# Performance work log

Measured on AMD Instinct MI355X. Metric: run time of the kernel, lower is better.

## Reference

```python
import jax, jax.numpy as jnp
import numpy as np

HIDDEN = 2048
N_HEADS = 16
Q_DIM = N_HEADS * 128  # 2048
INTER = 10944
EPS = 1e-6
B, S = 2, 2048


def rms_norm(x, w, eps):
    var = jnp.mean(jnp.square(x), axis=-1, keepdims=True)
    return x * jax.lax.rsqrt(var + eps) * w


def setup_inputs() -> dict:
    key = jax.random.key(0)
    ks = jax.random.split(key, 8)
    x = jax.random.normal(ks[0], (B, S, HIDDEN), dtype=jnp.float32)
    positions = jnp.broadcast_to(jnp.arange(S, dtype=jnp.int32), (B, S))
    sc = 0.02
    return {
        "x": x,
        "positions": positions,
        "in_w": jnp.ones((HIDDEN,), dtype=jnp.float32),
        "post_w": jnp.ones((HIDDEN,), dtype=jnp.float32),
        "Wq": jax.random.normal(ks[1], (Q_DIM, HIDDEN), dtype=jnp.float32) * sc,
        "Wo": jax.random.normal(ks[2], (HIDDEN, Q_DIM), dtype=jnp.float32) * sc,
        "Wg": jax.random.normal(ks[3], (INTER, HIDDEN), dtype=jnp.float32) * sc,
        "Wu": jax.random.normal(ks[4], (INTER, HIDDEN), dtype=jnp.float32) * sc,
        "Wd": jax.random.normal(ks[5], (HIDDEN, INTER), dtype=jnp.float32) * sc,
    }


def reference(x, positions, in_w, post_w, Wq, Wo, Wg, Wu, Wd):
    b, s, h = x.shape
    xf = x.reshape(-1, h)                       # [T, H]
    h_norm = rms_norm(xf, in_w, EPS)            # RMSNorm (input_layernorm)
    q = jnp.einsum('th,qh->tq', h_norm, Wq)     # q_proj
    hidden = xf + jnp.einsum('tq,hq->th', q, Wo)  # o_proj + residual
    h_post = rms_norm(hidden, post_w, EPS)      # post_attention_layernorm
    gate = jax.nn.silu(jnp.einsum('th,ih->ti', h_post, Wg))
    up = jnp.einsum('th,ih->ti', h_post, Wu)
    mlp = jnp.einsum('ti,hi->th', gate * up, Wd)  # down_proj
    return (hidden + mlp).reshape(b, s, h)
```

## Files before the change

kernel.cpp:

```cpp
#include <hip/hip_runtime.h>
#include <hip/hip_bf16.h>
#include <stdint.h>


typedef __bf16 bf16;
typedef bf16 bf16x8 __attribute__((ext_vector_type(8)));
typedef bf16 bf16x4 __attribute__((ext_vector_type(4)));
typedef float f32x4 __attribute__((ext_vector_type(4)));

#define HID     2048
#define TOK     4096
#define INTER   10944
#define INTER_P 11008
#define BK      32

__device__ __forceinline__ void gload_lds16(const bf16* g, bf16* l) {
    __builtin_amdgcn_global_load_lds(
        (const __attribute__((address_space(1))) void*)g,
        (__attribute__((address_space(3))) void*)l, 16, 0, 0);
}

__global__ __launch_bounds__(256) void conv_pad(const float* __restrict__ src,
                                                bf16* __restrict__ dst,
                                                int n_src, int n_dst) {
    int i = (blockIdx.x * 256 + threadIdx.x) * 4;
    if (i >= n_dst) return;
    float4 v = make_float4(0.f, 0.f, 0.f, 0.f);
    if (i < n_src) v = *(const float4*)(src + i);
    bf16x4 o;
    o[0] = (bf16)v.x; o[1] = (bf16)v.y; o[2] = (bf16)v.z; o[3] = (bf16)v.w;
    *(bf16x4*)(dst + i) = o;
}

__global__ __launch_bounds__(256) void conv_wd(const float* __restrict__ src,
                                               bf16* __restrict__ dst) {
    int i = (blockIdx.x * 256 + threadIdx.x) * 4;
    if (i >= HID * INTER_P) return;
    int row = i / INTER_P;
    int col = i - row * INTER_P;
    float4 v = make_float4(0.f, 0.f, 0.f, 0.f);
    if (col < INTER)
        v = *(const float4*)(src + (size_t)row * INTER + col);
    bf16x4 o;
    o[0] = (bf16)v.x; o[1] = (bf16)v.y; o[2] = (bf16)v.z; o[3] = (bf16)v.w;
    *(bf16x4*)(dst + i) = o;
}

__global__ __launch_bounds__(256) void rmsnorm_k(const float* __restrict__ x,
                                                 const float* __restrict__ w,
                                                 bf16* __restrict__ out) {
    const int row = blockIdx.x;
    const int tid = threadIdx.x;
    const float* xr = x + (size_t)row * HID + tid * 8;
    float4 v0 = *(const float4*)(xr);
    float4 v1 = *(const float4*)(xr + 4);
    float s = v0.x * v0.x + v0.y * v0.y + v0.z * v0.z + v0.w * v0.w +
              v1.x * v1.x + v1.y * v1.y + v1.z * v1.z + v1.w * v1.w;
    #pragma unroll
    for (int o = 32; o > 0; o >>= 1) s += __shfl_down(s, o);
    __shared__ float red[4];
    if ((tid & 63) == 0) red[tid >> 6] = s;
    __syncthreads();
    float tot = red[0] + red[1] + red[2] + red[3];
    float scale = rsqrtf(tot * (1.0f / (float)HID) + 1e-6f);
    float4 w0 = *(const float4*)(w + tid * 8);
    float4 w1 = *(const float4*)(w + tid * 8 + 4);
    bf16x8 o8;
    o8[0] = (bf16)(v0.x * scale * w0.x);
    o8[1] = (bf16)(v0.y * scale * w0.y);
    o8[2] = (bf16)(v0.z * scale * w0.z);
    o8[3] = (bf16)(v0.w * scale * w0.w);
    o8[4] = (bf16)(v1.x * scale * w1.x);
    o8[5] = (bf16)(v1.y * scale * w1.y);
    o8[6] = (bf16)(v1.z * scale * w1.z);
    o8[7] = (bf16)(v1.w * scale * w1.w);
    *(bf16x8*)(out + (size_t)row * HID + tid * 8) = o8;
}

template <int EPI>
__global__ __launch_bounds__(512, 4) void gemm_bt5(const bf16* __restrict__ A,
                                                   const bf16* __restrict__ W,
                                                   const float* __restrict__ res,
                                                   void* __restrict__ out,
                                                   int N, int K) {
    __shared__ bf16 lA[128 * BK];
    __shared__ bf16 lW[128 * BK];
    const int tid = threadIdx.x;
    const int rowBase = blockIdx.x * 128;
    const int colBase = blockIdx.y * 128;
    const int wave = tid >> 6, lane = tid & 63;
    const int wm = (wave >> 2) * 64, wn = (wave & 3) * 32;
    const int lr = lane & 15, kq = lane >> 4;

    f32x4 acc[4][2] = {};
    const bf16* Ab = A + (size_t)rowBase * K;
    const bf16* Wb = W + (size_t)colBase * K;

    const int sr = tid >> 2;
    const int ss = (tid & 3) ^ ((sr >> 1) & 3);
    const size_t goff = (size_t)sr * K + ss * 8;

    int aoff[4], woff[2];
    #pragma unroll
    for (int i = 0; i < 4; ++i) {
        int r = wm + i * 16 + lr;
        aoff[i] = r * BK + (kq ^ ((r >> 1) & 3)) * 8;
    }
    #pragma unroll
    for (int i = 0; i < 2; ++i) {
        int r = wn + i * 16 + lr;
        woff[i] = r * BK + (kq ^ ((r >> 1) & 3)) * 8;
    }

    for (int k0 = 0; k0 < K; k0 += BK) {
        gload_lds16(Ab + goff + k0, &lA[tid * 8]);
        gload_lds16(Wb + goff + k0, &lW[tid * 8]);
        __syncthreads();
        bf16x8 af[4], wf[2];
        #pragma unroll
        for (int i = 0; i < 4; ++i) af[i] = *(const bf16x8*)&lA[aoff[i]];
        #pragma unroll
        for (int i = 0; i < 2; ++i) wf[i] = *(const bf16x8*)&lW[woff[i]];
        #pragma unroll
        for (int mi = 0; mi < 4; ++mi)
            #pragma unroll
            for (int ni = 0; ni < 2; ++ni)
                acc[mi][ni] = __builtin_amdgcn_mfma_f32_16x16x32_bf16(
                    af[mi], wf[ni], acc[mi][ni], 0, 0, 0);
        __syncthreads();
    }
    const int rq = lane >> 4, cn = lane & 15;
    #pragma unroll
    for (int mi = 0; mi < 4; ++mi) {
        #pragma unroll
        for (int ni = 0; ni < 2; ++ni) {
            int col = colBase + wn + ni * 16 + cn;
            #pragma unroll
            for (int r = 0; r < 4; ++r) {
                int row = rowBase + wm + mi * 16 + rq * 4 + r;
                size_t idx = (size_t)row * N + col;
                float v = acc[mi][ni][r];
                if (EPI == 0) ((bf16*)out)[idx] = (bf16)v;
                else          ((float*)out)[idx] = res[idx] + v;
            }
        }
    }
}

__global__ __launch_bounds__(512, 4) void gemm_gu5(const bf16* __restrict__ A,
                                                   const bf16* __restrict__ Wg,
                                                   const bf16* __restrict__ Wu,
                                                   bf16* __restrict__ out,
                                                   int N, int K) {
    __shared__ bf16 lA[128 * BK];
    __shared__ bf16 lG[128 * BK];
    __shared__ bf16 lU[128 * BK];
    const int tid = threadIdx.x;
    const int rowBase = blockIdx.x * 128;
    const int colBase = blockIdx.y * 128;
    const int wave = tid >> 6, lane = tid & 63;
    const int wm = (wave >> 2) * 64, wn = (wave & 3) * 32;
    const int lr = lane & 15, kq = lane >> 4;

    f32x4 ag[4][2] = {};
    f32x4 au[4][2] = {};
    const bf16* Ab = A + (size_t)rowBase * K;
    const bf16* Gb = Wg + (size_t)colBase * K;
    const bf16* Ub = Wu + (size_t)colBase * K;

    const int sr = tid >> 2;
    const int ss = (tid & 3) ^ ((sr >> 1) & 3);
    const size_t goff = (size_t)sr * K + ss * 8;

    int aoff[4], boff[2];
    #pragma unroll
    for (int i = 0; i < 4; ++i) {
        int r = wm + i * 16 + lr;
        aoff[i] = r * BK + (kq ^ ((r >> 1) & 3)) * 8;
    }
    #pragma unroll
    for (int i = 0; i < 2; ++i) {
        int r = wn + i * 16 + lr;
        boff[i] = r * BK + (kq ^ ((r >> 1) & 3)) * 8;
    }

    for (int k0 = 0; k0 < K; k0 += BK) {
        gload_lds16(Ab + goff + k0, &lA[tid * 8]);
        gload_lds16(Gb + goff + k0, &lG[tid * 8]);
        gload_lds16(Ub + goff + k0, &lU[tid * 8]);
        __syncthreads();
        bf16x8 af[4], gf[2], uf[2];
        #pragma unroll
        for (int i = 0; i < 4; ++i) af[i] = *(const bf16x8*)&lA[aoff[i]];
        #pragma unroll
        for (int i = 0; i < 2; ++i) {
            gf[i] = *(const bf16x8*)&lG[boff[i]];
            uf[i] = *(const bf16x8*)&lU[boff[i]];
        }
        #pragma unroll
        for (int mi = 0; mi < 4; ++mi)
            #pragma unroll
            for (int ni = 0; ni < 2; ++ni) {
                ag[mi][ni] = __builtin_amdgcn_mfma_f32_16x16x32_bf16(
                    af[mi], gf[ni], ag[mi][ni], 0, 0, 0);
                au[mi][ni] = __builtin_amdgcn_mfma_f32_16x16x32_bf16(
                    af[mi], uf[ni], au[mi][ni], 0, 0, 0);
            }
        __syncthreads();
    }
    const int rq = lane >> 4, cn = lane & 15;
    #pragma unroll
    for (int mi = 0; mi < 4; ++mi) {
        #pragma unroll
        for (int ni = 0; ni < 2; ++ni) {
            int col = colBase + wn + ni * 16 + cn;
            #pragma unroll
            for (int r = 0; r < 4; ++r) {
                int row = rowBase + wm + mi * 16 + rq * 4 + r;
                float g = ag[mi][ni][r];
                float u = au[mi][ni][r];
                float sg = g / (1.0f + __expf(-g));
                out[(size_t)row * N + col] = (bf16)(sg * u);
            }
        }
    }
}

extern "C" void kernel_launch(void* const* d_in, const int* in_sizes, int n_in,
                              void* d_out, int out_size, void* d_ws, size_t ws_size,
                              hipStream_t stream) {
    const float* x      = (const float*)d_in[0];
    const float* in_w   = (const float*)d_in[2];
    const float* post_w = (const float*)d_in[3];
    const float* Wq     = (const float*)d_in[4];
    const float* Wo     = (const float*)d_in[5];
    const float* Wg     = (const float*)d_in[6];
    const float* Wu     = (const float*)d_in[7];
    const float* Wd     = (const float*)d_in[8];

    char* ws = (char*)d_ws;
    bf16*  X    = (bf16*)(ws + 0);
    bf16*  Yq   = (bf16*)(ws + 16777216);
    float* hid  = (float*)(ws + 33554432);
    bf16*  gu   = (bf16*)(ws + 67108864);
    bf16*  w0   = (bf16*)(ws + 157286400);
    bf16*  w1   = (bf16*)(ws + 202375168);
    bf16*  wsm  = (bf16*)(ws + 247463936);

    const int nGU  = INTER_P * HID;
    const int nGUs = INTER * HID;
    const int nSq  = HID * HID;

    conv_pad<<<nGU / 4 / 256, 256, 0, stream>>>(Wg, w0, nGUs, nGU);
    conv_pad<<<nGU / 4 / 256, 256, 0, stream>>>(Wu, w1, nGUs, nGU);
    conv_pad<<<nSq / 4 / 256, 256, 0, stream>>>(Wq, wsm, nSq, nSq);

    rmsnorm_k<<<TOK, 256, 0, stream>>>(x, in_w, X);
    gemm_bt5<0><<<dim3(TOK / 128, HID / 128), 512, 0, stream>>>(
        X, wsm, nullptr, Yq, HID, HID);
    conv_pad<<<nSq / 4 / 256, 256, 0, stream>>>(Wo, wsm, nSq, nSq);
    gemm_bt5<1><<<dim3(TOK / 128, HID / 128), 512, 0, stream>>>(
        Yq, wsm, x, hid, HID, HID);
    rmsnorm_k<<<TOK, 256, 0, stream>>>(hid, post_w, X);
    gemm_gu5<<<dim3(TOK / 128, INTER_P / 128), 512, 0, stream>>>(
        X, w0, w1, gu, INTER_P, HID);
    conv_wd<<<nGU / 4 / 256, 256, 0, stream>>>(Wd, w0);
    gemm_bt5<1><<<dim3(TOK / 128, HID / 128), 512, 0, stream>>>(
        gu, w0, hid, (float*)d_out, HID, INTER_P);
}
```

Baseline: 1.093 ms.

## Replace GEMMs with 256x256 double-buffered pipelined kernel plus split-K and combine passes

```diff
diff --git a/kernel.cpp b/kernel.cpp
--- a/kernel.cpp
+++ b/kernel.cpp
@@ -12,13 +12,19 @@
 #define TOK     4096
 #define INTER   10944
 #define INTER_P 11008
-#define BK      32
 
 __device__ __forceinline__ void gload_lds16(const bf16* g, bf16* l) {
     __builtin_amdgcn_global_load_lds(
         (const __attribute__((address_space(1))) void*)g,
         (__attribute__((address_space(3))) void*)l, 16, 0, 0);
 }
+
+#define SBAR()      asm volatile("s_barrier" ::: "memory")
+#define VMCNT(n)    asm volatile("s_waitcnt vmcnt(" #n ")" ::: "memory")
+#define LGKM(n)     asm volatile("s_waitcnt lgkmcnt(" #n ")" ::: "memory")
+#define SCHED0()    __builtin_amdgcn_sched_barrier(0)
+#define PRIO(n)     __builtin_amdgcn_s_setprio(n)
+#define FMA16(d, a, b) d = __builtin_amdgcn_mfma_f32_16x16x32_bf16(a, b, d, 0, 0, 0)
 
 __global__ __launch_bounds__(256) void conv_pad(const float* __restrict__ src,
                                                 bf16* __restrict__ dst,
@@ -77,151 +83,181 @@
     *(bf16x8*)(out + (size_t)row * HID + tid * 8) = o8;
 }
 
+#define BUFE 32768
+
 template <int EPI>
-__global__ __launch_bounds__(512, 4) void gemm_bt5(const bf16* __restrict__ A,
-                                                   const bf16* __restrict__ W,
-                                                   const float* __restrict__ res,
-                                                   void* __restrict__ out,
-                                                   int N, int K) {
-    __shared__ bf16 lA[128 * BK];
-    __shared__ bf16 lW[128 * BK];
+__global__ __launch_bounds__(512, 2) void gemm256(const bf16* __restrict__ A,
+                                                  const bf16* __restrict__ W,
+                                                  float* __restrict__ out0,
+                                                  float* __restrict__ out1,
+                                                  int N, int K, int ntz) {
+    extern __shared__ bf16 lds[];
     const int tid = threadIdx.x;
-    const int rowBase = blockIdx.x * 128;
-    const int colBase = blockIdx.y * 128;
+    const int rowBase = blockIdx.x * 256;
+    const int colBase = blockIdx.y * 256;
+    const int kt0 = blockIdx.z * ntz;
     const int wave = tid >> 6, lane = tid & 63;
-    const int wm = (wave >> 2) * 64, wn = (wave & 3) * 32;
-    const int lr = lane & 15, kq = lane >> 4;
-
-    f32x4 acc[4][2] = {};
-    const bf16* Ab = A + (size_t)rowBase * K;
-    const bf16* Wb = W + (size_t)colBase * K;
-
-    const int sr = tid >> 2;
-    const int ss = (tid & 3) ^ ((sr >> 1) & 3);
-    const size_t goff = (size_t)sr * K + ss * 8;
-
-    int aoff[4], woff[2];
+    const int wm = wave >> 2, wn = wave & 3;
+    const int fr = lane & 15, kq = lane >> 4;
+
+    const int slr = tid >> 3;
+    const int sc  = (tid & 7) ^ (slr & 7);
+    const bf16* sAb = A + (size_t)(rowBase + slr) * K + sc * 8;
+    const bf16* sWb = W + (size_t)(colBase + slr) * K + sc * 8;
+    const int ldst = tid * 8;
+
+    int aof[8][2], wof[4][2];
     #pragma unroll
-    for (int i = 0; i < 4; ++i) {
-        int r = wm + i * 16 + lr;
-        aoff[i] = r * BK + (kq ^ ((r >> 1) & 3)) * 8;
+    for (int mi = 0; mi < 8; ++mi) {
+        const int ra = mi * 32 + wm * 16 + fr;
+        #pragma unroll
+        for (int ks = 0; ks < 2; ++ks)
+            aof[mi][ks] = ra * 64 + (((ks * 4 + kq) ^ (ra & 7)) * 8);
     }
     #pragma unroll
-    for (int i = 0; i < 2; ++i) {
-        int r = wn + i * 16 + lr;
-        woff[i] = r * BK + (kq ^ ((r >> 1) & 3)) * 8;
+    for (int nj = 0; nj < 4; ++nj) {
+        const int rw = nj * 64 + wn * 16 + fr;
+        #pragma unroll
+        for (int ks = 0; ks < 2; ++ks)
+            wof[nj][ks] = 16384 + rw * 64 + (((ks * 4 + kq) ^ (rw & 7)) * 8);
     }
 
-    for (int k0 = 0; k0 < K; k0 += BK) {
-        gload_lds16(Ab + goff + k0, &lA[tid * 8]);
-        gload_lds16(Wb + goff + k0, &lW[tid * 8]);
-        __syncthreads();
-        bf16x8 af[4], wf[2];
-        #pragma unroll
-        for (int i = 0; i < 4; ++i) af[i] = *(const bf16x8*)&lA[aoff[i]];
-        #pragma unroll
-        for (int i = 0; i < 2; ++i) wf[i] = *(const bf16x8*)&lW[woff[i]];
-        #pragma unroll
-        for (int mi = 0; mi < 4; ++mi)
+    f32x4 acc[8][4] = {};
+
+#define STG(isA, hh, tt)                                                     \
+    do {                                                                     \
+        const bf16* _b = (isA) ? sAb : sWb;                                  \
+        bf16* _d = &lds[(((tt) & 1) * BUFE) + ((isA) ? 0 : 16384) +          \
+                        (hh) * 8192 + ldst];                                 \
+        const size_t _kb = (size_t)(kt0 + (tt)) * 64;                        \
+        gload_lds16(_b + (size_t)((hh) * 128) * K + _kb, _d);                \
+        gload_lds16(_b + (size_t)((hh) * 128 + 64) * K + _kb, _d + 4096);    \
+    } while (0)
+
+    STG(1, 0, 0); STG(0, 0, 0); STG(1, 1, 0); STG(0, 1, 0);
+    STG(1, 0, 1);
+    VMCNT(2);
+    SBAR();
+
+    for (int t = 0; t < ntz; ++t) {
+        const int bb = (t & 1) * BUFE;
+        const bool s1 = (t + 1) < ntz;
+        const bool s2 = (t + 2) < ntz;
+        bf16x8 aF[4][2], wF0[2][2], wF1[2][2];
+        if (s1) STG(0, 0, t + 1);
+        #pragma unroll
+        for (int m = 0; m < 4; ++m)
+          #pragma unroll
+          for (int ks = 0; ks < 2; ++ks)
+            aF[m][ks] = *(const bf16x8*)&lds[bb + aof[m][ks]];
+        #pragma unroll
+        for (int n = 0; n < 2; ++n)
+          #pragma unroll
+          for (int ks = 0; ks < 2; ++ks)
+            wF0[n][ks] = *(const bf16x8*)&lds[bb + wof[n][ks]];
+        LGKM(8);
+        SBAR(); LGKM(0); SCHED0();
+        PRIO(1);
+        #pragma unroll
+        for (int ks = 0; ks < 2; ++ks)
+          #pragma unroll
+          for (int m = 0; m < 4; ++m)
             #pragma unroll
-            for (int ni = 0; ni < 2; ++ni)
-                acc[mi][ni] = __builtin_amdgcn_mfma_f32_16x16x32_bf16(
-                    af[mi], wf[ni], acc[mi][ni], 0, 0, 0);
-        __syncthreads();
+            for (int n = 0; n < 2; ++n)
+                FMA16(acc[m][n], aF[m][ks], wF0[n][ks]);
+        PRIO(0); SCHED0(); SBAR();
+        if (s1) STG(1, 1, t + 1);
+        #pragma unroll
+        for (int n = 0; n < 2; ++n)
+          #pragma unroll
+          for (int ks = 0; ks < 2; ++ks)
+            wF1[n][ks] = *(const bf16x8*)&lds[bb + wof[2 + n][ks]];
+        SBAR(); LGKM(0); SCHED0();
+        PRIO(1);
+        #pragma unroll
+        for (int ks = 0; ks < 2; ++ks)
+          #pragma unroll
+          for (int m = 0; m < 4; ++m)
+            #pragma unroll
+            for (int n = 0; n < 2; ++n)
+                FMA16(acc[m][2 + n], aF[m][ks], wF1[n][ks]);
+        PRIO(0); SCHED0(); SBAR();
+        if (s1) STG(0, 1, t + 1);
+        #pragma unroll
+        for (int m = 0; m < 4; ++m)
+          #pragma unroll
+          for (int ks = 0; ks < 2; ++ks)
+            aF[m][ks] = *(const bf16x8*)&lds[bb + aof[4 + m][ks]];
+        SBAR(); LGKM(0); SCHED0();
+        PRIO(1);
+        #pragma unroll
+        for (int ks = 0; ks < 2; ++ks)
+          #pragma unroll
+          for (int m = 0; m < 4; ++m)
+            #pragma unroll
+            for (int n = 0; n < 2; ++n)
+                FMA16(acc[4 + m][2 + n], aF[m][ks], wF1[n][ks]);
+        PRIO(0); SCHED0(); SBAR();
+        if (s2) STG(1, 0, t + 2);
+        SCHED0();
+        PRIO(1);
+        #pragma unroll
+        for (int ks = 0; ks < 2; ++ks)
+          #pragma unroll
+          for (int m = 0; m < 4; ++m)
+            #pragma unroll
+            for (int n = 0; n < 2; ++n)
+                FMA16(acc[4 + m][n], aF[m][ks], wF0[n][ks]);
+        PRIO(0); SCHED0();
+        if (s2) VMCNT(2); else VMCNT(0);
+        SBAR();
     }
+#undef STG
     const int rq = lane >> 4, cn = lane & 15;
+    float* dst = blockIdx.z ? out1 : out0;
     #pragma unroll
-    for (int mi = 0; mi < 4; ++mi) {
-        #pragma unroll
-        for (int ni = 0; ni < 2; ++ni) {
-            int col = colBase + wn + ni * 16 + cn;
-            #pragma unroll
-            for (int r = 0; r < 4; ++r) {
-                int row = rowBase + wm + mi * 16 + rq * 4 + r;
-                size_t idx = (size_t)row * N + col;
-                float v = acc[mi][ni][r];
-                if (EPI == 0) ((bf16*)out)[idx] = (bf16)v;
-                else          ((float*)out)[idx] = res[idx] + v;
+    for (int mi = 0; mi < 8; ++mi)
+      #pragma unroll
+      for (int nj = 0; nj < 4; ++nj) {
+        const int col = colBase + nj * 64 + wn * 16 + cn;
+        #pragma unroll
+        for (int r = 0; r < 4; ++r) {
+            const int row = rowBase + mi * 32 + wm * 16 + rq * 4 + r;
+            const size_t idx = (size_t)row * N + col;
+            const float v = acc[mi][nj][r];
+            if (EPI == 0) {
+                dst[idx] = v;
+            } else if (EPI == 1) {
+                ((bf16*)out0)[idx] = (bf16)v;
+            } else {
+                bf16* p = (bf16*)out0;
+                const float u = (float)p[idx];
+                const float sg = v / (1.0f + __expf(-v));
+                p[idx] = (bf16)(sg * u);
             }
         }
-    }
-}
-
-__global__ __launch_bounds__(512, 4) void gemm_gu5(const bf16* __restrict__ A,
-                                                   const bf16* __restrict__ Wg,
-                                                   const bf16* __restrict__ Wu,
-                                                   bf16* __restrict__ out,
-                                                   int N, int K) {
-    __shared__ bf16 lA[128 * BK];
-    __shared__ bf16 lG[128 * BK];
-    __shared__ bf16 lU[128 * BK];
-    const int tid = threadIdx.x;
-    const int rowBase = blockIdx.x * 128;
-    const int colBase = blockIdx.y * 128;
-    const int wave = tid >> 6, lane = tid & 63;
-    const int wm = (wave >> 2) * 64, wn = (wave & 3) * 32;
-    const int lr = lane & 15, kq = lane >> 4;
-
-    f32x4 ag[4][2] = {};
-    f32x4 au[4][2] = {};
-    const bf16* Ab = A + (size_t)rowBase * K;
-    const bf16* Gb = Wg + (size_t)colBase * K;
-    const bf16* Ub = Wu + (size_t)colBase * K;
-
-    const int sr = tid >> 2;
-    const int ss = (tid & 3) ^ ((sr >> 1) & 3);
-    const size_t goff = (size_t)sr * K + ss * 8;
-
-    int aoff[4], boff[2];
-    #pragma unroll
-    for (int i = 0; i < 4; ++i) {
-        int r = wm + i * 16 + lr;
-        aoff[i] = r * BK + (kq ^ ((r >> 1) & 3)) * 8;
-    }
-    #pragma unroll
-    for (int i = 0; i < 2; ++i) {
-        int r = wn + i * 16 + lr;
-        boff[i] = r * BK + (kq ^ ((r >> 1) & 3)) * 8;
-    }
-
-    for (int k0 = 0; k0 < K; k0 += BK) {
-        gload_lds16(Ab + goff + k0, &lA[tid * 8]);
-        gload_lds16(Gb + goff + k0, &lG[tid * 8]);
-        gload_lds16(Ub + goff + k0, &lU[tid * 8]);
-        __syncthreads();
-        bf16x8 af[4], gf[2], uf[2];
-        #pragma unroll
-        for (int i = 0; i < 4; ++i) af[i] = *(const bf16x8*)&lA[aoff[i]];
-        #pragma unroll
-        for (int i = 0; i < 2; ++i) {
-            gf[i] = *(const bf16x8*)&lG[boff[i]];
-            uf[i] = *(const bf16x8*)&lU[boff[i]];
-        }
-        #pragma unroll
-        for (int mi = 0; mi < 4; ++mi)
-            #pragma unroll
-            for (int ni = 0; ni < 2; ++ni) {
-                ag[mi][ni] = __builtin_amdgcn_mfma_f32_16x16x32_bf16(
-                    af[mi], gf[ni], ag[mi][ni], 0, 0, 0);
-                au[mi][ni] = __builtin_amdgcn_mfma_f32_16x16x32_bf16(
-                    af[mi], uf[ni], au[mi][ni], 0, 0, 0);
-            }
-        __syncthreads();
-    }
-    const int rq = lane >> 4, cn = lane & 15;
-    #pragma unroll
-    for (int mi = 0; mi < 4; ++mi) {
-        #pragma unroll
-        for (int ni = 0; ni < 2; ++ni) {
-            int col = colBase + wn + ni * 16 + cn;
-            #pragma unroll
-            for (int r = 0; r < 4; ++r) {
-                int row = rowBase + wm + mi * 16 + rq * 4 + r;
-                float g = ag[mi][ni][r];
-                float u = au[mi][ni][r];
-                float sg = g / (1.0f + __expf(-g));
-                out[(size_t)row * N + col] = (bf16)(sg * u);
-            }
+      }
+}
+
+template <int MODE>
+__global__ __launch_bounds__(256) void combine_k(const float* __restrict__ p0,
+                                                 const float* __restrict__ p1,
+                                                 const float* __restrict__ res,
+                                                 void* __restrict__ out, int n) {
+    for (int i = (blockIdx.x * 256 + threadIdx.x) * 4; i < n;
+         i += gridDim.x * 1024) {
+        float4 a = *(const float4*)(p0 + i);
+        float4 b = *(const float4*)(p1 + i);
+        float4 v = make_float4(a.x + b.x, a.y + b.y, a.z + b.z, a.w + b.w);
+        if (MODE == 1) {
+            float4 r = *(const float4*)(res + i);
+            v.x += r.x; v.y += r.y; v.z += r.z; v.w += r.w;
+            *(float4*)((float*)out + i) = v;
+        } else {
+            bf16x4 o;
+            o[0] = (bf16)v.x; o[1] = (bf16)v.y;
+            o[2] = (bf16)v.z; o[3] = (bf16)v.w;
+            *(bf16x4*)((bf16*)out + i) = o;
         }
     }
 }
@@ -238,6 +274,14 @@
     const float* Wu     = (const float*)d_in[7];
     const float* Wd     = (const float*)d_in[8];
 
+    const int LDSB = 2 * BUFE * 2;
+    hipFuncSetAttribute(reinterpret_cast<const void*>(&gemm256<0>),
+                        hipFuncAttributeMaxDynamicSharedMemorySize, LDSB);
+    hipFuncSetAttribute(reinterpret_cast<const void*>(&gemm256<1>),
+                        hipFuncAttributeMaxDynamicSharedMemorySize, LDSB);
+    hipFuncSetAttribute(reinterpret_cast<const void*>(&gemm256<2>),
+                        hipFuncAttributeMaxDynamicSharedMemorySize, LDSB);
+
     char* ws = (char*)d_ws;
     bf16*  X    = (bf16*)(ws + 0);
     bf16*  Yq   = (bf16*)(ws + 16777216);
@@ -246,25 +290,35 @@
     bf16*  w0   = (bf16*)(ws + 157286400);
     bf16*  w1   = (bf16*)(ws + 202375168);
     bf16*  wsm  = (bf16*)(ws + 247463936);
+    float* qp0  = (float*)(ws + 67108864);
+    float* qp1  = (float*)(ws + 100663296);
+    float* dp0  = (float*)(ws + 202375168);
+    float* dp1  = (float*)(ws + 0);
 
     const int nGU  = INTER_P * HID;
     const int nGUs = INTER * HID;
     const int nSq  = HID * HID;
+    const int nTH  = TOK * HID;
 
     conv_pad<<<nGU / 4 / 256, 256, 0, stream>>>(Wg, w0, nGUs, nGU);
     conv_pad<<<nGU / 4 / 256, 256, 0, stream>>>(Wu, w1, nGUs, nGU);
     conv_pad<<<nSq / 4 / 256, 256, 0, stream>>>(Wq, wsm, nSq, nSq);
 
     rmsnorm_k<<<TOK, 256, 0, stream>>>(x, in_w, X);
-    gemm_bt5<0><<<dim3(TOK / 128, HID / 128), 512, 0, stream>>>(
-        X, wsm, nullptr, Yq, HID, HID);
+    gemm256<0><<<dim3(TOK / 256, HID / 256, 2), 512, LDSB, stream>>>(
+        X, wsm, qp0, qp1, HID, HID, 16);
+    combine_k<0><<<2048, 256, 0, stream>>>(qp0, qp1, nullptr, Yq, nTH);
     conv_pad<<<nSq / 4 / 256, 256, 0, stream>>>(Wo, wsm, nSq, nSq);
-    gemm_bt5<1><<<dim3(TOK / 128, HID / 128), 512, 0, stream>>>(
-        Yq, wsm, x, hid, HID, HID);
+    gemm256<0><<<dim3(TOK / 256, HID / 256, 2), 512, LDSB, stream>>>(
+        Yq, wsm, qp0, qp1, HID, HID, 16);
+    combine_k<1><<<2048, 256, 0, stream>>>(qp0, qp1, x, hid, nTH);
     rmsnorm_k<<<TOK, 256, 0, stream>>>(hid, post_w, X);
-    gemm_gu5<<<dim3(TOK / 128, INTER_P / 128), 512, 0, stream>>>(
-        X, w0, w1, gu, INTER_P, HID);
+    gemm256<1><<<dim3(TOK / 256, INTER_P / 256, 1), 512, LDSB, stream>>>(
+        X, w1, (float*)gu, nullptr, INTER_P, HID, 32);
+    gemm256<2><<<dim3(TOK / 256, INTER_P / 256, 1), 512, LDSB, stream>>>(
+        X, w0, (float*)gu, nullptr, INTER_P, HID, 32);
     conv_wd<<<nGU / 4 / 256, 256, 0, stream>>>(Wd, w0);
-    gemm_bt5<1><<<dim3(TOK / 128, HID / 128), 512, 0, stream>>>(
-        gu, w0, hid, (float*)d_out, HID, INTER_P);
-}
+    gemm256<0><<<dim3(TOK / 256, HID / 256, 2), 512, LDSB, stream>>>(
+        gu, w0, dp0, dp1, HID, INTER_P, 86);
+    combine_k<1><<<2048, 256, 0, stream>>>(dp0, dp1, hid, (float*)d_out, nTH);
+}
```

New measurement: 1.142 ms. 4.4% more time.
